# Kernel tuning notes

Measured on AMD Instinct MI355X. Metric: run time of the kernel, lower is better.

## Reference

```python
import jax, jax.numpy as jnp
import numpy as np

B, NUM_RX, NUM_CHIRPS, SAMPLES = 16, 4, 64, 256
D_BINS, R_BINS = 64, 256


def _conv3d(x, w, b, pad):
    y = jax.lax.conv_general_dilated(x, w, (1, 1, 1), pad,
                                     dimension_numbers=('NCDHW', 'OIDHW', 'NCDHW'))
    return y + b[None, :, None, None, None]


def _conv2d(x, w, b, pad):
    y = jax.lax.conv_general_dilated(x, w, (1, 1), pad,
                                     dimension_numbers=('NCHW', 'OIHW', 'NCHW'))
    return y + b[None, :, None, None]


def _bn2(x, s, t):
    return x * s[None, :, None, None] + t[None, :, None, None]


def _bn3(x, s, t):
    return x * s[None, :, None, None, None] + t[None, :, None, None, None]


def _upsample_bilinear_ac(x, oh, ow):
    # torch Upsample(mode='bilinear', align_corners=True)
    _, _, h, w = x.shape
    ph = jnp.linspace(0.0, h - 1.0, oh)
    pw = jnp.linspace(0.0, w - 1.0, ow)
    h0 = jnp.clip(jnp.floor(ph).astype(jnp.int32), 0, h - 1)
    h1 = jnp.clip(h0 + 1, 0, h - 1)
    fh = ph - h0
    w0 = jnp.clip(jnp.floor(pw).astype(jnp.int32), 0, w - 1)
    w1 = jnp.clip(w0 + 1, 0, w - 1)
    fw = pw - w0
    x = x[:, :, h0, :] * (1.0 - fh)[None, None, :, None] + x[:, :, h1, :] * fh[None, None, :, None]
    x = x[:, :, :, w0] * (1.0 - fw) + x[:, :, :, w1] * fw
    return x


def setup_inputs() -> dict:
    ks = iter(jax.random.split(jax.random.key(0), 80))

    def nrm(shape, s=0.05):
        return s * jax.random.normal(next(ks), shape, dtype=jnp.float32)

    inp = {'x': jax.random.normal(next(ks), (B, NUM_RX, NUM_CHIRPS, SAMPLES, 2), dtype=jnp.float32)}

    def conv(name, shape):
        inp[name + '_w'] = nrm(shape)
        inp[name + '_b'] = nrm((shape[0],))

    def bn(name, n):  # BatchNorm in inference form folded to scale/shift
        inp[name + '_s'] = 1.0 + nrm((n,), 0.1)
        inp[name + '_t'] = nrm((n,), 0.1)

    conv('tc1', (16, 2, 1, 1, 3)); bn('tc1', 16)
    conv('tc2', (32, 16, 1, 1, 3)); bn('tc2', 32)
    conv('rx', (32, 32, NUM_RX, 1, 1)); bn('rx', 32)
    conv('cc1', (64, 32 * NUM_CHIRPS, 3, 3)); bn('cc1', 64)
    conv('cc2', (64, 64, 3, 3)); bn('cc2', 64)
    conv('rd1', (128, 64, 3, 3)); bn('rd1', 128)
    conv('rd2', (128, 128, 3, 3)); bn('rd2', 128)
    conv('up1', (64, 128, 3, 3)); bn('up1', 64)
    conv('up2', (32, 64, 3, 3)); bn('up2', 32)
    conv('up3', (1, 32, 1, 1))
    inp['wr'] = jax.random.normal(next(ks), (SAMPLES, R_BINS, 2), dtype=jnp.float32)
    inp['wd'] = jax.random.normal(next(ks), (NUM_CHIRPS, D_BINS, 2), dtype=jnp.float32)
    return inp


def reference(x, tc1_w, tc1_b, tc1_s, tc1_t, tc2_w, tc2_b, tc2_s, tc2_t,
              rx_w, rx_b, rx_s, rx_t, cc1_w, cc1_b, cc1_s, cc1_t,
              cc2_w, cc2_b, cc2_s, cc2_t, rd1_w, rd1_b, rd1_s, rd1_t,
              rd2_w, rd2_b, rd2_s, rd2_t, up1_w, up1_b, up1_s, up1_t,
              up2_w, up2_b, up2_s, up2_t, up3_w, up3_b, wr, wd):
    r = jax.nn.relu
    p3 = [(0, 0), (0, 0), (1, 1)]
    p2 = [(1, 1), (1, 1)]
    h = jnp.transpose(x, (0, 4, 1, 2, 3))                      # [B,2,RX,C,S]
    h = r(_bn3(_conv3d(h, tc1_w, tc1_b, p3), tc1_s, tc1_t))
    h = r(_bn3(_conv3d(h, tc2_w, tc2_b, p3), tc2_s, tc2_t))
    h = r(_bn3(_conv3d(h, rx_w, rx_b, [(0, 0)] * 3), rx_s, rx_t))[:, :, 0]  # [B,32,C,S]
    h = h.reshape(h.shape[0], -1, SAMPLES)[:, :, None, :]      # [B,32*C,1,S]
    h = r(_bn2(_conv2d(h, cc1_w, cc1_b, p2), cc1_s, cc1_t))
    h = r(_bn2(_conv2d(h, cc2_w, cc2_b, p2), cc2_s, cc2_t))
    h = r(_bn2(_conv2d(h, rd1_w, rd1_b, p2), rd1_s, rd1_t))
    h = r(_bn2(_conv2d(h, rd2_w, rd2_b, p2), rd2_s, rd2_t))
    h = _upsample_bilinear_ac(h, D_BINS, R_BINS)               # [B,128,D,R]
    h = r(_bn2(_conv2d(h, up1_w, up1_b, p2), up1_s, up1_t))
    h = r(_bn2(_conv2d(h, up2_w, up2_b, p2), up2_s, up2_t))
    h = jax.nn.sigmoid(_conv2d(h, up3_w, up3_b, [(0, 0), (0, 0)]))  # [B,1,D,R]
    # learnable_fft (input is real: x_imag = 0), loops -> two batched matmuls
    xr = h[:, 0]                                               # [B,D,R]
    rr = jnp.einsum('bcs,sr->bcr', xr, wr[:, :, 0])            # range DFT, real
    ri = jnp.einsum('bcs,sr->bcr', xr, wr[:, :, 1])            # range DFT, imag
    rdr = jnp.einsum('bcr,cd->bdr', rr, wd[:, :, 0]) - jnp.einsum('bcr,cd->bdr', ri, wd[:, :, 1])
    rdi = jnp.einsum('bcr,cd->bdr', rr, wd[:, :, 1]) + jnp.einsum('bcr,cd->bdr', ri, wd[:, :, 0])
    mag = jnp.sqrt(rdr * rdr + rdi * rdi) / (NUM_CHIRPS * SAMPLES)
    out = jnp.clip(h + 0.1 * mag[:, None], 0.0, 1.0)
    return jnp.transpose(out, (0, 2, 3, 1))                    # [B,D,R,1]
```

## Files before the change

kernel.cpp:

```cpp
#include <hip/hip_runtime.h>
#include <math.h>

#define OFF_A      0u
#define OFF_P      8388608u
#define OFF_WCC1   10485760u
#define OFF_BCC1   11010048u
#define OFF_WCC2   11010112u
#define OFF_BCC2   11026496u
#define OFF_WRD1   11026560u
#define OFF_BRD1   11059328u
#define OFF_WRD2   11059456u
#define OFF_BRD2   11124992u
#define OFF_WUP1   11125120u
#define OFF_BUP1   11223424u
#define OFF_WUP2   11223488u
#define OFF_BUP2   11346368u
#define OFF_WRX    11346400u
#define OFF_W1F    11350496u
#define OFF_B1F    11350592u
#define OFF_W2F    11350608u
#define OFF_B2F    11352144u
#define OFF_BRXF   11352176u
#define OFF_R      0u
#define OFF_U1     524288u
#define OFF_H      1310720u

__device__ __forceinline__ void fma4(float4& a, const float4& x, float w) {
  a.x = fmaf(x.x, w, a.x); a.y = fmaf(x.y, w, a.y);
  a.z = fmaf(x.z, w, a.z); a.w = fmaf(x.w, w, a.w);
}

__global__ __launch_bounds__(256) void k_repack(
    const float* __restrict__ tc1_w, const float* __restrict__ tc1_b, const float* __restrict__ tc1_s, const float* __restrict__ tc1_t,
    const float* __restrict__ tc2_w, const float* __restrict__ tc2_b, const float* __restrict__ tc2_s, const float* __restrict__ tc2_t,
    const float* __restrict__ rx_w, const float* __restrict__ rx_b, const float* __restrict__ rx_s, const float* __restrict__ rx_t,
    const float* __restrict__ cc1_w, const float* __restrict__ cc1_b, const float* __restrict__ cc1_s, const float* __restrict__ cc1_t,
    const float* __restrict__ cc2_w, const float* __restrict__ cc2_b, const float* __restrict__ cc2_s, const float* __restrict__ cc2_t,
    const float* __restrict__ rd1_w, const float* __restrict__ rd1_b, const float* __restrict__ rd1_s, const float* __restrict__ rd1_t,
    const float* __restrict__ rd2_w, const float* __restrict__ rd2_b, const float* __restrict__ rd2_s, const float* __restrict__ rd2_t,
    const float* __restrict__ up1_w, const float* __restrict__ up1_b, const float* __restrict__ up1_s, const float* __restrict__ up1_t,
    const float* __restrict__ up2_w, const float* __restrict__ up2_b, const float* __restrict__ up2_s, const float* __restrict__ up2_t,
    float* __restrict__ ws)
{
  const int tid = blockIdx.x * blockDim.x + threadIdx.x;
  const int nth = gridDim.x * blockDim.x;

  for (int i = tid; i < 96; i += nth) ws[OFF_W1F + i] = tc1_w[i] * tc1_s[i/6];
  for (int i = tid; i < 16; i += nth) ws[OFF_B1F + i] = tc1_b[i]*tc1_s[i] + tc1_t[i];
  for (int i = tid; i < 1536; i += nth) {
    int oc = i & 31, r = i >> 5, k = r % 3, ic = r / 3;
    ws[OFF_W2F + i] = tc2_w[oc*48 + ic*3 + k] * tc2_s[oc];
  }
  for (int i = tid; i < 32; i += nth) ws[OFF_B2F + i] = tc2_b[i]*tc2_s[i] + tc2_t[i];
  for (int i = tid; i < 4096; i += nth) {
    int oc = i & 31, ic = (i >> 5) & 31, rxi = i >> 10;
    ws[OFF_WRX + i] = rx_w[(oc*32 + ic)*4 + rxi] * rx_s[oc];
  }
  for (int i = tid; i < 32; i += nth) ws[OFF_BRXF + i] = rx_b[i]*rx_s[i] + rx_t[i];

  for (int i = tid; i < 2048*64*4; i += nth) {
    int k = i & 3, oc = (i >> 2) & 63, c2 = i >> 8;
    ws[OFF_WCC1 + i] = (k < 3) ? cc1_w[((oc*2048 + c2)*3 + 1)*3 + k] * cc1_s[oc] : 0.f;
  }
  for (int i = tid; i < 64; i += nth) ws[OFF_BCC1 + i] = cc1_b[i]*cc1_s[i] + cc1_t[i];

  for (int i = tid; i < 64*64*4; i += nth) {
    int k = i & 3, oc = (i >> 2) & 63, ic = i >> 8;
    ws[OFF_WCC2 + i] = (k < 3) ? cc2_w[((oc*64 + ic)*3 + 1)*3 + k] * cc2_s[oc] : 0.f;
  }
  for (int i = tid; i < 64; i += nth) ws[OFF_BCC2 + i] = cc2_b[i]*cc2_s[i] + cc2_t[i];

  for (int i = tid; i < 64*128*4; i += nth) {
    int k = i & 3, oc = (i >> 2) & 127, ic = i >> 9;
    ws[OFF_WRD1 + i] = (k < 3) ? rd1_w[((oc*64 + ic)*3 + 1)*3 + k] * rd1_s[oc] : 0.f;
  }
  for (int i = tid; i < 128; i += nth) ws[OFF_BRD1 + i] = rd1_b[i]*rd1_s[i] + rd1_t[i];

  for (int i = tid; i < 128*128*4; i += nth) {
    int k = i & 3, oc = (i >> 2) & 127, ic = i >> 9;
    ws[OFF_WRD2 + i] = (k < 3) ? rd2_w[((oc*128 + ic)*3 + 1)*3 + k] * rd2_s[oc] : 0.f;
  }
  for (int i = tid; i < 128; i += nth) ws[OFF_BRD2 + i] = rd2_b[i]*rd2_s[i] + rd2_t[i];

  for (int i = tid; i < 3*128*64*4; i += nth) {
    int k = i & 3, oc = (i >> 2) & 63, ic = (i >> 8) & 127, v = i >> 15;
    float val = 0.f;
    if (k < 3) {
      const int m = (v == 0) ? 6 : (v == 1) ? 7 : 3;
      float a = 0.f;
      for (int kh = 0; kh < 3; ++kh)
        if ((m >> kh) & 1) a += up1_w[((oc*128 + ic)*3 + kh)*3 + k];
      val = a * up1_s[oc];
    }
    ws[OFF_WUP1 + i] = val;
  }
  for (int i = tid; i < 64; i += nth) ws[OFF_BUP1 + i] = up1_b[i]*up1_s[i] + up1_t[i];

  for (int i = tid; i < 5*3*64*32*4; i += nth) {
    int k = i & 3, oc = (i >> 2) & 31, ic = (i >> 7) & 63, t = i >> 13;
    int src = t % 3, v = t / 3;
    float val = 0.f;
    if (k < 3) {
      const int MASKS[15] = {2,4,0,  1,6,0,  0,7,0,  0,3,4,  0,1,2};
      const int m = MASKS[v*3 + src];
      float a = 0.f;
      for (int kh = 0; kh < 3; ++kh)
        if ((m >> kh) & 1) a += up2_w[((oc*64 + ic)*3 + kh)*3 + k];
      val = a * up2_s[oc];
    }
    ws[OFF_WUP2 + i] = val;
  }
  for (int i = tid; i < 32; i += nth) ws[OFF_BUP2 + i] = up2_b[i]*up2_s[i] + up2_t[i];
}

__global__ __launch_bounds__(256, 4) void k_front(
    const float* __restrict__ x, const float* __restrict__ ws, float* __restrict__ A)
{
  __shared__ float t1s[16][258];
  const int tid = threadIdx.x;
  const int b = blockIdx.x >> 6, chirp = blockIdx.x & 63;
  const int s = tid;

  if (tid < 32) { int o = tid & 15; int c = (tid >> 4) ? 257 : 0; t1s[o][c] = 0.f; }

  const float* w1f  = ws + OFF_W1F;
  const float* b1f  = ws + OFF_B1F;
  const float* w2f  = ws + OFF_W2F;
  const float* b2f  = ws + OFF_B2F;
  const float* wrxf = ws + OFF_WRX;
  const float* brxf = ws + OFF_BRXF;

  float acc[32];
  #pragma unroll
  for (int j = 0; j < 32; ++j) acc[j] = 0.f;

  #pragma unroll 1
  for (int rxi = 0; rxi < 4; ++rxi) {
    {
      const float2* xb2 = (const float2*)(x + ((size_t)(((b*4 + rxi)*64 + chirp)*256) << 1));
      float2 xm = xb2[s];
      float2 xl = xb2[(s == 0) ? 0 : (s - 1)];
      float2 xr = xb2[(s == 255) ? 255 : (s + 1)];
      if (s == 0)   { xl.x = 0.f; xl.y = 0.f; }
      if (s == 255) { xr.x = 0.f; xr.y = 0.f; }
      #pragma unroll 4
      for (int o = 0; o < 16; ++o) {
        const float* w = w1f + o*6;
        float v = b1f[o];
        v = fmaf(xl.x, w[0], v);
        v = fmaf(xm.x, w[1], v);
        v = fmaf(xr.x, w[2], v);
        v = fmaf(xl.y, w[3], v);
        v = fmaf(xm.y, w[4], v);
        v = fmaf(xr.y, w[5], v);
        t1s[o][s+1] = fmaxf(v, 0.f);
      }
    }
    __syncthreads();

    float t2[32];
    #pragma unroll
    for (int j = 0; j < 32; ++j) t2[j] = b2f[j];
    #pragma unroll 2
    for (int ic = 0; ic < 16; ++ic) {
      float tl = t1s[ic][s];
      float tm = t1s[ic][s+1];
      float tr = t1s[ic][s+2];
      const float* w = w2f + ic*96;
      #pragma unroll
      for (int oc = 0; oc < 32; ++oc)
        t2[oc] = fmaf(tl, w[oc], fmaf(tm, w[32+oc], fmaf(tr, w[64+oc], t2[oc])));
    }
    #pragma unroll
    for (int j = 0; j < 32; ++j) t2[j] = fmaxf(t2[j], 0.f);

    const float* wr0 = wrxf + rxi*1024;
    #pragma unroll 4
    for (int ic = 0; ic < 32; ++ic) {
      float tv = t2[ic];
      const float* w = wr0 + ic*32;
      #pragma unroll
      for (int oc = 0; oc < 32; ++oc)
        acc[oc] = fmaf(tv, w[oc], acc[oc]);
    }
    __syncthreads();
  }

  #pragma unroll 4
  for (int oc = 0; oc < 32; ++oc) {
    float v = fmaxf(acc[oc] + brxf[oc], 0.f);
    A[(size_t)((b*2048 + oc*64 + chirp)*256) + s] = v;
  }
}

__global__ __launch_bounds__(256) void k_cc1(
    const float* __restrict__ A, const float* __restrict__ wp, float* __restrict__ P)
{
  __shared__ __align__(16) float As[256][36];
  const int tid = threadIdx.x;
  const int ks = blockIdx.x & 7;
  const int stile = (blockIdx.x >> 3) & 7;
  const int b = blockIdx.x >> 6;
  const int s0 = stile * 32;
  const int oc = tid & 63;
  const int sg = tid >> 6;
  const int cbase = ks * 256;
  const float4* w4 = (const float4*)wp;

  for (int i = tid; i < 256*36; i += 256) {
    int c = i / 36, si = i - c*36;
    int sA = s0 - 1 + si;
    float v = 0.f;
    if (si < 34 && sA >= 0 && sA < 256)
      v = A[(size_t)(b*2048 + cbase + c)*256 + sA];
    As[c][si] = v;
  }
  __syncthreads();

  const int sb = sg * 8;
  float4 acc0 = make_float4(0.f,0.f,0.f,0.f);
  float4 acc1 = make_float4(0.f,0.f,0.f,0.f);
  #pragma unroll 4
  for (int c = 0; c < 256; ++c) {
    float4 w = w4[(size_t)(cbase + c)*64 + oc];
    float4 a0 = *(const float4*)&As[c][sb];
    float4 a1 = *(const float4*)&As[c][sb + 4];
    float2 a2 = *(const float2*)&As[c][sb + 8];
    acc0.x = fmaf(a0.x,w.x, fmaf(a0.y,w.y, fmaf(a0.z,w.z, acc0.x)));
    acc0.y = fmaf(a0.y,w.x, fmaf(a0.z,w.y, fmaf(a0.w,w.z, acc0.y)));
    acc0.z = fmaf(a0.z,w.x, fmaf(a0.w,w.y, fmaf(a1.x,w.z, acc0.z)));
    acc0.w = fmaf(a0.w,w.x, fmaf(a1.x,w.y, fmaf(a1.y,w.z, acc0.w)));
    acc1.x = fmaf(a1.x,w.x, fmaf(a1.y,w.y, fmaf(a1.z,w.z, acc1.x)));
    acc1.y = fmaf(a1.y,w.x, fmaf(a1.z,w.y, fmaf(a1.w,w.z, acc1.y)));
    acc1.z = fmaf(a1.z,w.x, fmaf(a1.w,w.y, fmaf(a2.x,w.z, acc1.z)));
    acc1.w = fmaf(a1.w,w.x, fmaf(a2.x,w.y, fmaf(a2.y,w.z, acc1.w)));
  }
  float* Pk = P + ((size_t)(ks*16 + b)*256)*64;
  int s = s0 + sb;
  Pk[(size_t)(s+0)*64 + oc] = acc0.x;
  Pk[(size_t)(s+1)*64 + oc] = acc0.y;
  Pk[(size_t)(s+2)*64 + oc] = acc0.z;
  Pk[(size_t)(s+3)*64 + oc] = acc0.w;
  Pk[(size_t)(s+4)*64 + oc] = acc1.x;
  Pk[(size_t)(s+5)*64 + oc] = acc1.y;
  Pk[(size_t)(s+6)*64 + oc] = acc1.z;
  Pk[(size_t)(s+7)*64 + oc] = acc1.w;
}

__global__ __launch_bounds__(256) void k_mid(
    const float* __restrict__ P, const float* __restrict__ bcc1,
    const float* __restrict__ wcc2, const float* __restrict__ bcc2,
    const float* __restrict__ wrd1, const float* __restrict__ brd1,
    const float* __restrict__ wrd2, const float* __restrict__ brd2,
    float* __restrict__ R)
{
  __shared__ float c1s[14][64];
  __shared__ float c2s[14][64];
  __shared__ float r1s[10][128];
  const int tid = threadIdx.x;
  const int b = blockIdx.x >> 5;
  const int s0 = (blockIdx.x & 31) * 8;
  const float4* wc2 = (const float4*)wcc2;
  const float4* wr1 = (const float4*)wrd1;
  const float4* wr2 = (const float4*)wrd2;

  for (int i = tid; i < 14*64; i += 256) {
    int si = i >> 6, ic = i & 63;
    int sA = s0 - 3 + si;
    float v = 0.f;
    if (sA >= 0 && sA < 256) {
      float a = bcc1[ic];
      #pragma unroll
      for (int ksp = 0; ksp < 8; ++ksp)
        a += P[((size_t)(ksp*16 + b)*256 + sA)*64 + ic];
      v = fmaxf(a, 0.f);
    }
    c1s[si][ic] = v;
  }
  __syncthreads();

  {
    const int g = tid >> 6, oc = tid & 63;
    if (g < 3) {
      float4 acc;
      float bb = bcc2[oc];
      acc = make_float4(bb, bb, bb, bb);
      for (int ic = 0; ic < 64; ++ic) {
        float4 w = wc2[ic*64 + oc];
        float c0 = c1s[g*4+0][ic], c1 = c1s[g*4+1][ic], c2 = c1s[g*4+2][ic];
        float c3 = c1s[g*4+3][ic], c4 = c1s[g*4+4][ic], c5 = c1s[g*4+5][ic];
        acc.x = fmaf(c0,w.x, fmaf(c1,w.y, fmaf(c2,w.z, acc.x)));
        acc.y = fmaf(c1,w.x, fmaf(c2,w.y, fmaf(c3,w.z, acc.y)));
        acc.z = fmaf(c2,w.x, fmaf(c3,w.y, fmaf(c4,w.z, acc.z)));
        acc.w = fmaf(c3,w.x, fmaf(c4,w.y, fmaf(c5,w.z, acc.w)));
      }
      c2s[g*4+0][oc] = fmaxf(acc.x, 0.f);
      c2s[g*4+1][oc] = fmaxf(acc.y, 0.f);
      c2s[g*4+2][oc] = fmaxf(acc.z, 0.f);
      c2s[g*4+3][oc] = fmaxf(acc.w, 0.f);
    } else {
      int k = tid - 192;
      c2s[12][k] = 0.f;
      c2s[13][k] = 0.f;
    }
  }
  __syncthreads();

  for (int it = tid; it < 384; it += 256) {
    const int oc = it & 127, g = it >> 7;
    float4 acc;
    float bb = brd1[oc];
    acc = make_float4(bb, bb, bb, bb);
    for (int ic = 0; ic < 64; ++ic) {
      float4 w = wr1[ic*128 + oc];
      float c0 = c2s[g*4+0][ic], c1 = c2s[g*4+1][ic], c2 = c2s[g*4+2][ic];
      float c3 = c2s[g*4+3][ic], c4 = c2s[g*4+4][ic], c5 = c2s[g*4+5][ic];
      acc.x = fmaf(c0,w.x, fmaf(c1,w.y, fmaf(c2,w.z, acc.x)));
      acc.y = fmaf(c1,w.x, fmaf(c2,w.y, fmaf(c3,w.z, acc.y)));
      acc.z = fmaf(c2,w.x, fmaf(c3,w.y, fmaf(c4,w.z, acc.z)));
      acc.w = fmaf(c3,w.x, fmaf(c4,w.y, fmaf(c5,w.z, acc.w)));
    }
    r1s[g*4+0][oc] = fmaxf(acc.x, 0.f);
    r1s[g*4+1][oc] = fmaxf(acc.y, 0.f);
    if (g < 2) {
      r1s[g*4+2][oc] = fmaxf(acc.z, 0.f);
      r1s[g*4+3][oc] = fmaxf(acc.w, 0.f);
    }
  }
  __syncthreads();

  {
    const int g = tid >> 7, oc = tid & 127;
    float4 acc;
    float bb = brd2[oc];
    acc = make_float4(bb, bb, bb, bb);
    for (int ic = 0; ic < 128; ++ic) {
      float4 w = wr2[ic*128 + oc];
      float c0 = r1s[g*4+0][ic], c1 = r1s[g*4+1][ic], c2 = r1s[g*4+2][ic];
      float c3 = r1s[g*4+3][ic], c4 = r1s[g*4+4][ic], c5 = r1s[g*4+5][ic];
      acc.x = fmaf(c0,w.x, fmaf(c1,w.y, fmaf(c2,w.z, acc.x)));
      acc.y = fmaf(c1,w.x, fmaf(c2,w.y, fmaf(c3,w.z, acc.y)));
      acc.z = fmaf(c2,w.x, fmaf(c3,w.y, fmaf(c4,w.z, acc.z)));
      acc.w = fmaf(c3,w.x, fmaf(c4,w.y, fmaf(c5,w.z, acc.w)));
    }
    int s = s0 + g*4;
    R[((size_t)b*256 + s+0)*128 + oc] = fmaxf(acc.x, 0.f);
    R[((size_t)b*256 + s+1)*128 + oc] = fmaxf(acc.y, 0.f);
    R[((size_t)b*256 + s+2)*128 + oc] = fmaxf(acc.z, 0.f);
    R[((size_t)b*256 + s+3)*128 + oc] = fmaxf(acc.w, 0.f);
  }
}

__global__ __launch_bounds__(192) void k_up1(
    const float* __restrict__ R, const float* __restrict__ wup1, const float* __restrict__ bup1,
    float* __restrict__ U1)
{
  __shared__ float Rs[10][128];
  const int tid = threadIdx.x;
  const int b = blockIdx.x >> 5;
  const int s0 = (blockIdx.x & 31) * 8;
  for (int i = tid; i < 10*128; i += 192) {
    int si = i >> 7, ic = i & 127;
    int sA = s0 - 1 + si;
    Rs[si][ic] = (sA >= 0 && sA < 256) ? R[((size_t)b*256 + sA)*128 + ic] : 0.f;
  }
  __syncthreads();
  const int vi = tid >> 6, oc = tid & 63;
  const float4* w4 = (const float4*)wup1;
  float acc[8];
  float bb = bup1[oc];
  #pragma unroll
  for (int j = 0; j < 8; ++j) acc[j] = bb;
  for (int ic = 0; ic < 128; ++ic) {
    float4 w = w4[(vi*128 + ic)*64 + oc];
    float r0 = Rs[0][ic], r1 = Rs[1][ic], r2 = Rs[2][ic], r3 = Rs[3][ic], r4 = Rs[4][ic];
    float r5 = Rs[5][ic], r6 = Rs[6][ic], r7 = Rs[7][ic], r8 = Rs[8][ic], r9 = Rs[9][ic];
    acc[0] = fmaf(r0,w.x, fmaf(r1,w.y, fmaf(r2,w.z, acc[0])));
    acc[1] = fmaf(r1,w.x, fmaf(r2,w.y, fmaf(r3,w.z, acc[1])));
    acc[2] = fmaf(r2,w.x, fmaf(r3,w.y, fmaf(r4,w.z, acc[2])));
    acc[3] = fmaf(r3,w.x, fmaf(r4,w.y, fmaf(r5,w.z, acc[3])));
    acc[4] = fmaf(r4,w.x, fmaf(r5,w.y, fmaf(r6,w.z, acc[4])));
    acc[5] = fmaf(r5,w.x, fmaf(r6,w.y, fmaf(r7,w.z, acc[5])));
    acc[6] = fmaf(r6,w.x, fmaf(r7,w.y, fmaf(r8,w.z, acc[6])));
    acc[7] = fmaf(r7,w.x, fmaf(r8,w.y, fmaf(r9,w.z, acc[7])));
  }
  #pragma unroll
  for (int j = 0; j < 8; ++j)
    U1[((size_t)(b*3 + vi)*256 + s0 + j)*64 + oc] = fmaxf(acc[j], 0.f);
}

__global__ __launch_bounds__(192) void k_up2(
    const float* __restrict__ U1, const float* __restrict__ wup2, const float* __restrict__ bup2,
    const float* __restrict__ up3_w, const float* __restrict__ up3_b,
    float* __restrict__ H)
{
  __shared__ float u1s[3][10][64];
  __shared__ float u2s[5][32][9];
  const int tid = threadIdx.x;
  const int b = blockIdx.x >> 5;
  const int s0 = (blockIdx.x & 31) * 8;
  for (int i = tid; i < 3*10*64; i += 192) {
    int v = i / 640, r = i - v*640, si = r >> 6, ic = r & 63;
    int sA = s0 - 1 + si;
    u1s[v][si][ic] = (sA >= 0 && sA < 256) ? U1[((size_t)(b*3 + v)*256 + sA)*64 + ic] : 0.f;
  }
  __syncthreads();
  if (tid < 160) {
    const int v = tid >> 5, oc = tid & 31;
    const float4* w4 = (const float4*)wup2;
    float acc[8];
    float bb = bup2[oc];
    #pragma unroll
    for (int j = 0; j < 8; ++j) acc[j] = bb;
    for (int src = 0; src < 3; ++src)
      for (int ic = 0; ic < 64; ++ic) {
        float4 w = w4[((v*3 + src)*64 + ic)*32 + oc];
        float r0 = u1s[src][0][ic], r1 = u1s[src][1][ic], r2 = u1s[src][2][ic];
        float r3 = u1s[src][3][ic], r4 = u1s[src][4][ic], r5 = u1s[src][5][ic];
        float r6 = u1s[src][6][ic], r7 = u1s[src][7][ic], r8 = u1s[src][8][ic];
        float r9 = u1s[src][9][ic];
        acc[0] = fmaf(r0,w.x, fmaf(r1,w.y, fmaf(r2,w.z, acc[0])));
        acc[1] = fmaf(r1,w.x, fmaf(r2,w.y, fmaf(r3,w.z, acc[1])));
        acc[2] = fmaf(r2,w.x, fmaf(r3,w.y, fmaf(r4,w.z, acc[2])));
        acc[3] = fmaf(r3,w.x, fmaf(r4,w.y, fmaf(r5,w.z, acc[3])));
        acc[4] = fmaf(r4,w.x, fmaf(r5,w.y, fmaf(r6,w.z, acc[4])));
        acc[5] = fmaf(r5,w.x, fmaf(r6,w.y, fmaf(r7,w.z, acc[5])));
        acc[6] = fmaf(r6,w.x, fmaf(r7,w.y, fmaf(r8,w.z, acc[6])));
        acc[7] = fmaf(r7,w.x, fmaf(r8,w.y, fmaf(r9,w.z, acc[7])));
      }
    #pragma unroll
    for (int j = 0; j < 8; ++j) u2s[v][oc][j] = fmaxf(acc[j], 0.f);
  }
  __syncthreads();
  if (tid < 40) {
    int v = tid >> 3, j = tid & 7;
    float a = up3_b[0];
    for (int ic = 0; ic < 32; ++ic)
      a = fmaf(u2s[v][ic][j], up3_w[ic], a);
    H[(size_t)(b*5 + v)*256 + s0 + j] = 1.f / (1.f + expf(-a));
  }
}

__global__ __launch_bounds__(64) void k_spec(
    const float* __restrict__ H, const float* __restrict__ wr, const float* __restrict__ wd,
    float* __restrict__ out)
{
  __shared__ float hs[5][256];
  __shared__ float S0[64], S1[64];
  __shared__ float wds[4][64][2];
  const int tid = threadIdx.x;
  const int b = blockIdx.x >> 2;
  const int rt = blockIdx.x & 3;
  for (int i = tid; i < 1280; i += 64) hs[i >> 8][i & 255] = H[(size_t)b*1280 + i];
  {
    float a0 = 0.f, a1 = 0.f;
    for (int c = 2; c <= 61; ++c) {
      a0 += wd[(c*64 + tid)*2 + 0];
      a1 += wd[(c*64 + tid)*2 + 1];
    }
    S0[tid] = a0; S1[tid] = a1;
  }
  for (int i = tid; i < 512; i += 64) {
    int row = i >> 7, rem = i & 127, d = rem >> 1, comp = rem & 1;
    int c = (row < 2) ? row : (60 + row);
    wds[row][d][comp] = wd[(c*64 + d)*2 + comp];
  }
  __syncthreads();
  const int r = rt*64 + tid;
  float rr0=0,rr1=0,rr2=0,rr3=0,rr4=0, ri0=0,ri1=0,ri2=0,ri3=0,ri4=0;
  const float2* wr2p = (const float2*)wr;
  for (int s = 0; s < 256; ++s) {
    float2 w = wr2p[s*256 + r];
    float h0 = hs[0][s], h1 = hs[1][s], h2 = hs[2][s], h3 = hs[3][s], h4 = hs[4][s];
    rr0 = fmaf(h0, w.x, rr0); ri0 = fmaf(h0, w.y, ri0);
    rr1 = fmaf(h1, w.x, rr1); ri1 = fmaf(h1, w.y, ri1);
    rr2 = fmaf(h2, w.x, rr2); ri2 = fmaf(h2, w.y, ri2);
    rr3 = fmaf(h3, w.x, rr3); ri3 = fmaf(h3, w.y, ri3);
    rr4 = fmaf(h4, w.x, rr4); ri4 = fmaf(h4, w.y, ri4);
  }
  for (int d = 0; d < 64; ++d) {
    float w0r = wds[0][d][0], w0i = wds[0][d][1];
    float w1r = wds[1][d][0], w1i = wds[1][d][1];
    float w2r = wds[2][d][0], w2i = wds[2][d][1];
    float w3r = wds[3][d][0], w3i = wds[3][d][1];
    float s0v = S0[d], s1v = S1[d];
    float rdr = rr0*w0r + rr1*w1r + rr2*s0v + rr3*w2r + rr4*w3r
              - ri0*w0i - ri1*w1i - ri2*s1v - ri3*w2i - ri4*w3i;
    float rdi = rr0*w0i + rr1*w1i + rr2*s1v + rr3*w2i + rr4*w3i
              + ri0*w0r + ri1*w1r + ri2*s0v + ri3*w2r + ri4*w3r;
    float mag = sqrtf(rdr*rdr + rdi*rdi) * (1.0f / 16384.0f);
    int v = (d == 0) ? 0 : (d == 1) ? 1 : (d <= 61) ? 2 : ((d == 62) ? 3 : 4);
    float o = hs[v][r] + 0.1f * mag;
    out[(size_t)b*16384 + d*256 + r] = fminf(fmaxf(o, 0.f), 1.f);
  }
}

extern "C" void kernel_launch(void* const* d_in, const int* in_sizes, int n_in,
                              void* d_out, int out_size, void* d_ws, size_t ws_size,
                              hipStream_t stream)
{
  const float* x     = (const float*)d_in[0];
  const float* tc1_w = (const float*)d_in[1];  const float* tc1_b = (const float*)d_in[2];
  const float* tc1_s = (const float*)d_in[3];  const float* tc1_t = (const float*)d_in[4];
  const float* tc2_w = (const float*)d_in[5];  const float* tc2_b = (const float*)d_in[6];
  const float* tc2_s = (const float*)d_in[7];  const float* tc2_t = (const float*)d_in[8];
  const float* rx_w  = (const float*)d_in[9];  const float* rx_b  = (const float*)d_in[10];
  const float* rx_s  = (const float*)d_in[11]; const float* rx_t  = (const float*)d_in[12];
  const float* cc1_w = (const float*)d_in[13]; const float* cc1_b = (const float*)d_in[14];
  const float* cc1_s = (const float*)d_in[15]; const float* cc1_t = (const float*)d_in[16];
  const float* cc2_w = (const float*)d_in[17]; const float* cc2_b = (const float*)d_in[18];
  const float* cc2_s = (const float*)d_in[19]; const float* cc2_t = (const float*)d_in[20];
  const float* rd1_w = (const float*)d_in[21]; const float* rd1_b = (const float*)d_in[22];
  const float* rd1_s = (const float*)d_in[23]; const float* rd1_t = (const float*)d_in[24];
  const float* rd2_w = (const float*)d_in[25]; const float* rd2_b = (const float*)d_in[26];
  const float* rd2_s = (const float*)d_in[27]; const float* rd2_t = (const float*)d_in[28];
  const float* up1_w = (const float*)d_in[29]; const float* up1_b = (const float*)d_in[30];
  const float* up1_s = (const float*)d_in[31]; const float* up1_t = (const float*)d_in[32];
  const float* up2_w = (const float*)d_in[33]; const float* up2_b = (const float*)d_in[34];
  const float* up2_s = (const float*)d_in[35]; const float* up2_t = (const float*)d_in[36];
  const float* up3_w = (const float*)d_in[37]; const float* up3_b = (const float*)d_in[38];
  const float* wr    = (const float*)d_in[39];
  const float* wd    = (const float*)d_in[40];
  float* ws  = (float*)d_ws;
  float* out = (float*)d_out;

  k_repack<<<1024, 256, 0, stream>>>(tc1_w, tc1_b, tc1_s, tc1_t,
                                     tc2_w, tc2_b, tc2_s, tc2_t,
                                     rx_w, rx_b, rx_s, rx_t,
                                     cc1_w, cc1_b, cc1_s, cc1_t,
                                     cc2_w, cc2_b, cc2_s, cc2_t,
                                     rd1_w, rd1_b, rd1_s, rd1_t,
                                     rd2_w, rd2_b, rd2_s, rd2_t,
                                     up1_w, up1_b, up1_s, up1_t,
                                     up2_w, up2_b, up2_s, up2_t, ws);
  k_front<<<1024, 256, 0, stream>>>(x, ws, ws + OFF_A);
  k_cc1<<<1024, 256, 0, stream>>>(ws + OFF_A, ws + OFF_WCC1, ws + OFF_P);
  k_mid<<<512, 256, 0, stream>>>(ws + OFF_P, ws + OFF_BCC1,
                                 ws + OFF_WCC2, ws + OFF_BCC2,
                                 ws + OFF_WRD1, ws + OFF_BRD1,
                                 ws + OFF_WRD2, ws + OFF_BRD2, ws + OFF_R);
  k_up1<<<512, 192, 0, stream>>>(ws + OFF_R, ws + OFF_WUP1, ws + OFF_BUP1, ws + OFF_U1);
  k_up2<<<512, 192, 0, stream>>>(ws + OFF_U1, ws + OFF_WUP2, ws + OFF_BUP2, up3_w, up3_b, ws + OFF_H);
  k_spec<<<64, 64, 0, stream>>>(ws + OFF_H, wr, wd, out);
}
```

Measured before the change: 392.7 us.

## Restructure front, cc1, mid, up and spectral kernels; fuse up1/up2

Several kernels are reworked together. k_front splits each chirp across two 128-thread blocks with halo recompute. k_cc1 drops the padded weight layout, moves to 128 threads each computing 4 positions by 4 output channels, and writes float4 stores. k_mid transposes its shared tiles so activations load as vectors. k_up1 and k_up2 are fused into one kernel that keeps the intermediate in shared memory, removing a launch and a global round trip. k_spec goes to 256 threads, splitting the range DFT over sample quarters with a shared-memory reduction, to raise parallelism in the tail kernel. In exchange these add more shared memory, extra halo work and new code paths that risk errors.

```diff
diff --git a/kernel.cpp b/kernel.cpp
--- a/kernel.cpp
+++ b/kernel.cpp
@@ -4,26 +4,25 @@
 #define OFF_A      0u
 #define OFF_P      8388608u
 #define OFF_WCC1   10485760u
-#define OFF_BCC1   11010048u
-#define OFF_WCC2   11010112u
-#define OFF_BCC2   11026496u
-#define OFF_WRD1   11026560u
-#define OFF_BRD1   11059328u
-#define OFF_WRD2   11059456u
-#define OFF_BRD2   11124992u
-#define OFF_WUP1   11125120u
-#define OFF_BUP1   11223424u
-#define OFF_WUP2   11223488u
-#define OFF_BUP2   11346368u
-#define OFF_WRX    11346400u
-#define OFF_W1F    11350496u
-#define OFF_B1F    11350592u
-#define OFF_W2F    11350608u
-#define OFF_B2F    11352144u
-#define OFF_BRXF   11352176u
+#define OFF_BCC1   10878976u
+#define OFF_WCC2   10879040u
+#define OFF_BCC2   10895424u
+#define OFF_WRD1   10895488u
+#define OFF_BRD1   10928256u
+#define OFF_WRD2   10928384u
+#define OFF_BRD2   10993920u
+#define OFF_WUP1   10994048u
+#define OFF_BUP1   11092352u
+#define OFF_WUP2   11092416u
+#define OFF_BUP2   11215296u
+#define OFF_WRX    11215328u
+#define OFF_W1F    11219424u
+#define OFF_B1F    11219520u
+#define OFF_W2F    11219536u
+#define OFF_B2F    11221072u
+#define OFF_BRXF   11221104u
 #define OFF_R      0u
-#define OFF_U1     524288u
-#define OFF_H      1310720u
+#define OFF_H      524288u
 
 __device__ __forceinline__ void fma4(float4& a, const float4& x, float w) {
   a.x = fmaf(x.x, w, a.x); a.y = fmaf(x.y, w, a.y);
@@ -58,70 +57,88 @@
   }
   for (int i = tid; i < 32; i += nth) ws[OFF_BRXF + i] = rx_b[i]*rx_s[i] + rx_t[i];
 
-  for (int i = tid; i < 2048*64*4; i += nth) {
-    int k = i & 3, oc = (i >> 2) & 63, c2 = i >> 8;
-    ws[OFF_WCC1 + i] = (k < 3) ? cc1_w[((oc*2048 + c2)*3 + 1)*3 + k] * cc1_s[oc] : 0.f;
+  for (int i = tid; i < 2048*192; i += nth) {
+    int c = i / 192, r = i - c*192, k = r >> 6, oc = r & 63;
+    ws[OFF_WCC1 + i] = cc1_w[((oc*2048 + c)*3 + 1)*3 + k] * cc1_s[oc];
   }
   for (int i = tid; i < 64; i += nth) ws[OFF_BCC1 + i] = cc1_b[i]*cc1_s[i] + cc1_t[i];
 
-  for (int i = tid; i < 64*64*4; i += nth) {
-    int k = i & 3, oc = (i >> 2) & 63, ic = i >> 8;
-    ws[OFF_WCC2 + i] = (k < 3) ? cc2_w[((oc*64 + ic)*3 + 1)*3 + k] * cc2_s[oc] : 0.f;
+  for (int i = tid; i < 64*64; i += nth) {
+    int oc = i & 63, ic = i >> 6;
+    float4 v;
+    v.x = cc2_w[(oc*64 + ic)*9 + 3] * cc2_s[oc];
+    v.y = cc2_w[(oc*64 + ic)*9 + 4] * cc2_s[oc];
+    v.z = cc2_w[(oc*64 + ic)*9 + 5] * cc2_s[oc];
+    v.w = 0.f;
+    ((float4*)(ws + OFF_WCC2))[i] = v;
   }
   for (int i = tid; i < 64; i += nth) ws[OFF_BCC2 + i] = cc2_b[i]*cc2_s[i] + cc2_t[i];
 
-  for (int i = tid; i < 64*128*4; i += nth) {
-    int k = i & 3, oc = (i >> 2) & 127, ic = i >> 9;
-    ws[OFF_WRD1 + i] = (k < 3) ? rd1_w[((oc*64 + ic)*3 + 1)*3 + k] * rd1_s[oc] : 0.f;
+  for (int i = tid; i < 64*128; i += nth) {
+    int oc = i & 127, ic = i >> 7;
+    float4 v;
+    v.x = rd1_w[(oc*64 + ic)*9 + 3] * rd1_s[oc];
+    v.y = rd1_w[(oc*64 + ic)*9 + 4] * rd1_s[oc];
+    v.z = rd1_w[(oc*64 + ic)*9 + 5] * rd1_s[oc];
+    v.w = 0.f;
+    ((float4*)(ws + OFF_WRD1))[i] = v;
   }
   for (int i = tid; i < 128; i += nth) ws[OFF_BRD1 + i] = rd1_b[i]*rd1_s[i] + rd1_t[i];
 
-  for (int i = tid; i < 128*128*4; i += nth) {
-    int k = i & 3, oc = (i >> 2) & 127, ic = i >> 9;
-    ws[OFF_WRD2 + i] = (k < 3) ? rd2_w[((oc*128 + ic)*3 + 1)*3 + k] * rd2_s[oc] : 0.f;
+  for (int i = tid; i < 128*128; i += nth) {
+    int oc = i & 127, ic = i >> 7;
+    float4 v;
+    v.x = rd2_w[(oc*128 + ic)*9 + 3] * rd2_s[oc];
+    v.y = rd2_w[(oc*128 + ic)*9 + 4] * rd2_s[oc];
+    v.z = rd2_w[(oc*128 + ic)*9 + 5] * rd2_s[oc];
+    v.w = 0.f;
+    ((float4*)(ws + OFF_WRD2))[i] = v;
   }
   for (int i = tid; i < 128; i += nth) ws[OFF_BRD2 + i] = rd2_b[i]*rd2_s[i] + rd2_t[i];
 
-  for (int i = tid; i < 3*128*64*4; i += nth) {
-    int k = i & 3, oc = (i >> 2) & 63, ic = (i >> 8) & 127, v = i >> 15;
-    float val = 0.f;
-    if (k < 3) {
-      const int m = (v == 0) ? 6 : (v == 1) ? 7 : 3;
-      float a = 0.f;
-      for (int kh = 0; kh < 3; ++kh)
-        if ((m >> kh) & 1) a += up1_w[((oc*128 + ic)*3 + kh)*3 + k];
-      val = a * up1_s[oc];
-    }
-    ws[OFF_WUP1 + i] = val;
+  for (int i = tid; i < 3*128*64; i += nth) {
+    int oc = i & 63, ic = (i >> 6) & 127, v = i >> 13;
+    const int m = (v == 0) ? 6 : (v == 1) ? 7 : 3;
+    float4 o = make_float4(0.f, 0.f, 0.f, 0.f);
+    for (int kh = 0; kh < 3; ++kh)
+      if ((m >> kh) & 1) {
+        o.x += up1_w[((oc*128 + ic)*3 + kh)*3 + 0];
+        o.y += up1_w[((oc*128 + ic)*3 + kh)*3 + 1];
+        o.z += up1_w[((oc*128 + ic)*3 + kh)*3 + 2];
+      }
+    o.x *= up1_s[oc]; o.y *= up1_s[oc]; o.z *= up1_s[oc];
+    ((float4*)(ws + OFF_WUP1))[i] = o;
   }
   for (int i = tid; i < 64; i += nth) ws[OFF_BUP1 + i] = up1_b[i]*up1_s[i] + up1_t[i];
 
-  for (int i = tid; i < 5*3*64*32*4; i += nth) {
-    int k = i & 3, oc = (i >> 2) & 31, ic = (i >> 7) & 63, t = i >> 13;
+  for (int i = tid; i < 5*3*64*32; i += nth) {
+    int oc = i & 31, ic = (i >> 5) & 63, t = i >> 11;
     int src = t % 3, v = t / 3;
-    float val = 0.f;
-    if (k < 3) {
-      const int MASKS[15] = {2,4,0,  1,6,0,  0,7,0,  0,3,4,  0,1,2};
-      const int m = MASKS[v*3 + src];
-      float a = 0.f;
-      for (int kh = 0; kh < 3; ++kh)
-        if ((m >> kh) & 1) a += up2_w[((oc*64 + ic)*3 + kh)*3 + k];
-      val = a * up2_s[oc];
-    }
-    ws[OFF_WUP2 + i] = val;
+    const int MASKS[15] = {2,4,0,  1,6,0,  0,7,0,  0,3,4,  0,1,2};
+    const int m = MASKS[v*3 + src];
+    float4 o = make_float4(0.f, 0.f, 0.f, 0.f);
+    for (int kh = 0; kh < 3; ++kh)
+      if ((m >> kh) & 1) {
+        o.x += up2_w[((oc*64 + ic)*3 + kh)*3 + 0];
+        o.y += up2_w[((oc*64 + ic)*3 + kh)*3 + 1];
+        o.z += up2_w[((oc*64 + ic)*3 + kh)*3 + 2];
+      }
+    o.x *= up2_s[oc]; o.y *= up2_s[oc]; o.z *= up2_s[oc];
+    ((float4*)(ws + OFF_WUP2))[i] = o;
   }
   for (int i = tid; i < 32; i += nth) ws[OFF_BUP2 + i] = up2_b[i]*up2_s[i] + up2_t[i];
 }
 
-__global__ __launch_bounds__(256, 4) void k_front(
+__global__ __launch_bounds__(128, 4) void k_front(
     const float* __restrict__ x, const float* __restrict__ ws, float* __restrict__ A)
 {
-  __shared__ float t1s[16][258];
+  __shared__ float t1s[16][132];
   const int tid = threadIdx.x;
-  const int b = blockIdx.x >> 6, chirp = blockIdx.x & 63;
-  const int s = tid;
-
-  if (tid < 32) { int o = tid & 15; int c = (tid >> 4) ? 257 : 0; t1s[o][c] = 0.f; }
+  const int b = blockIdx.x >> 7;
+  const int chirp = (blockIdx.x >> 1) & 63;
+  const int h = blockIdx.x & 1;
+  const int hs0 = h << 7;
+  const int s = hs0 + tid;
 
   const float* w1f  = ws + OFF_W1F;
   const float* b1f  = ws + OFF_B1F;
@@ -136,24 +153,28 @@
 
   #pragma unroll 1
   for (int rxi = 0; rxi < 4; ++rxi) {
-    {
-      const float2* xb2 = (const float2*)(x + ((size_t)(((b*4 + rxi)*64 + chirp)*256) << 1));
-      float2 xm = xb2[s];
-      float2 xl = xb2[(s == 0) ? 0 : (s - 1)];
-      float2 xr = xb2[(s == 255) ? 255 : (s + 1)];
-      if (s == 0)   { xl.x = 0.f; xl.y = 0.f; }
-      if (s == 255) { xr.x = 0.f; xr.y = 0.f; }
-      #pragma unroll 4
-      for (int o = 0; o < 16; ++o) {
-        const float* w = w1f + o*6;
-        float v = b1f[o];
-        v = fmaf(xl.x, w[0], v);
-        v = fmaf(xm.x, w[1], v);
-        v = fmaf(xr.x, w[2], v);
-        v = fmaf(xl.y, w[3], v);
-        v = fmaf(xm.y, w[4], v);
-        v = fmaf(xr.y, w[5], v);
-        t1s[o][s+1] = fmaxf(v, 0.f);
+    const float2* xb2 = (const float2*)(x + ((size_t)(((b*4 + rxi)*64 + chirp)*256) << 1));
+    for (int j = tid; j < 130; j += 128) {
+      int sc = hs0 - 1 + j;
+      if (sc < 0 || sc > 255) {
+        #pragma unroll
+        for (int o = 0; o < 16; ++o) t1s[o][j] = 0.f;
+      } else {
+        float2 xm = xb2[sc];
+        float2 xl = (sc == 0)   ? make_float2(0.f, 0.f) : xb2[sc-1];
+        float2 xr = (sc == 255) ? make_float2(0.f, 0.f) : xb2[sc+1];
+        #pragma unroll 4
+        for (int o = 0; o < 16; ++o) {
+          const float* w = w1f + o*6;
+          float v = b1f[o];
+          v = fmaf(xl.x, w[0], v);
+          v = fmaf(xm.x, w[1], v);
+          v = fmaf(xr.x, w[2], v);
+          v = fmaf(xl.y, w[3], v);
+          v = fmaf(xm.y, w[4], v);
+          v = fmaf(xr.y, w[5], v);
+          t1s[o][j] = fmaxf(v, 0.f);
+        }
       }
     }
     __syncthreads();
@@ -163,9 +184,9 @@
     for (int j = 0; j < 32; ++j) t2[j] = b2f[j];
     #pragma unroll 2
     for (int ic = 0; ic < 16; ++ic) {
-      float tl = t1s[ic][s];
-      float tm = t1s[ic][s+1];
-      float tr = t1s[ic][s+2];
+      float tl = t1s[ic][tid];
+      float tm = t1s[ic][tid+1];
+      float tr = t1s[ic][tid+2];
       const float* w = w2f + ic*96;
       #pragma unroll
       for (int oc = 0; oc < 32; ++oc)
@@ -193,7 +214,7 @@
   }
 }
 
-__global__ __launch_bounds__(256) void k_cc1(
+__global__ __launch_bounds__(128) void k_cc1(
     const float* __restrict__ A, const float* __restrict__ wp, float* __restrict__ P)
 {
   __shared__ __align__(16) float As[256][36];
@@ -202,12 +223,12 @@
   const int stile = (blockIdx.x >> 3) & 7;
   const int b = blockIdx.x >> 6;
   const int s0 = stile * 32;
-  const int oc = tid & 63;
-  const int sg = tid >> 6;
+  const int ocq = tid & 15;
+  const int sg = tid >> 4;
+  const int sb = sg * 4;
   const int cbase = ks * 256;
-  const float4* w4 = (const float4*)wp;
-
-  for (int i = tid; i < 256*36; i += 256) {
+
+  for (int i = tid; i < 256*36; i += 128) {
     int c = i / 36, si = i - c*36;
     int sA = s0 - 1 + si;
     float v = 0.f;
@@ -217,34 +238,28 @@
   }
   __syncthreads();
 
-  const int sb = sg * 8;
-  float4 acc0 = make_float4(0.f,0.f,0.f,0.f);
-  float4 acc1 = make_float4(0.f,0.f,0.f,0.f);
+  float4 acc[4];
+  #pragma unroll
+  for (int j = 0; j < 4; ++j) acc[j] = make_float4(0.f,0.f,0.f,0.f);
+
+  const float4* w4 = (const float4*)wp;
   #pragma unroll 4
   for (int c = 0; c < 256; ++c) {
-    float4 w = w4[(size_t)(cbase + c)*64 + oc];
+    const float4* wc = w4 + (size_t)(cbase + c)*48 + ocq;
+    float4 wk0 = wc[0];
+    float4 wk1 = wc[16];
+    float4 wk2 = wc[32];
     float4 a0 = *(const float4*)&As[c][sb];
-    float4 a1 = *(const float4*)&As[c][sb + 4];
-    float2 a2 = *(const float2*)&As[c][sb + 8];
-    acc0.x = fmaf(a0.x,w.x, fmaf(a0.y,w.y, fmaf(a0.z,w.z, acc0.x)));
-    acc0.y = fmaf(a0.y,w.x, fmaf(a0.z,w.y, fmaf(a0.w,w.z, acc0.y)));
-    acc0.z = fmaf(a0.z,w.x, fmaf(a0.w,w.y, fmaf(a1.x,w.z, acc0.z)));
-    acc0.w = fmaf(a0.w,w.x, fmaf(a1.x,w.y, fmaf(a1.y,w.z, acc0.w)));
-    acc1.x = fmaf(a1.x,w.x, fmaf(a1.y,w.y, fmaf(a1.z,w.z, acc1.x)));
-    acc1.y = fmaf(a1.y,w.x, fmaf(a1.z,w.y, fmaf(a1.w,w.z, acc1.y)));
-    acc1.z = fmaf(a1.z,w.x, fmaf(a1.w,w.y, fmaf(a2.x,w.z, acc1.z)));
-    acc1.w = fmaf(a1.w,w.x, fmaf(a2.x,w.y, fmaf(a2.y,w.z, acc1.w)));
+    float2 a1 = *(const float2*)&As[c][sb + 4];
+    fma4(acc[0], wk0, a0.x); fma4(acc[0], wk1, a0.y); fma4(acc[0], wk2, a0.z);
+    fma4(acc[1], wk0, a0.y); fma4(acc[1], wk1, a0.z); fma4(acc[1], wk2, a0.w);
+    fma4(acc[2], wk0, a0.z); fma4(acc[2], wk1, a0.w); fma4(acc[2], wk2, a1.x);
+    fma4(acc[3], wk0, a0.w); fma4(acc[3], wk1, a1.x); fma4(acc[3], wk2, a1.y);
   }
   float* Pk = P + ((size_t)(ks*16 + b)*256)*64;
-  int s = s0 + sb;
-  Pk[(size_t)(s+0)*64 + oc] = acc0.x;
-  Pk[(size_t)(s+1)*64 + oc] = acc0.y;
-  Pk[(size_t)(s+2)*64 + oc] = acc0.z;
-  Pk[(size_t)(s+3)*64 + oc] = acc0.w;
-  Pk[(size_t)(s+4)*64 + oc] = acc1.x;
-  Pk[(size_t)(s+5)*64 + oc] = acc1.y;
-  Pk[(size_t)(s+6)*64 + oc] = acc1.z;
-  Pk[(size_t)(s+7)*64 + oc] = acc1.w;
+  #pragma unroll
+  for (int j = 0; j < 4; ++j)
+    *(float4*)&Pk[(size_t)(s0 + sb + j)*64 + ocq*4] = acc[j];
 }
 
 __global__ __launch_bounds__(256) void k_mid(
@@ -254,9 +269,9 @@
     const float* __restrict__ wrd2, const float* __restrict__ brd2,
     float* __restrict__ R)
 {
-  __shared__ float c1s[14][64];
-  __shared__ float c2s[14][64];
-  __shared__ float r1s[10][128];
+  __shared__ __align__(16) float c1s[64][20];
+  __shared__ __align__(16) float c2s[64][20];
+  __shared__ __align__(16) float r1s[128][12];
   const int tid = threadIdx.x;
   const int b = blockIdx.x >> 5;
   const int s0 = (blockIdx.x & 31) * 8;
@@ -264,8 +279,8 @@
   const float4* wr1 = (const float4*)wrd1;
   const float4* wr2 = (const float4*)wrd2;
 
-  for (int i = tid; i < 14*64; i += 256) {
-    int si = i >> 6, ic = i & 63;
+  for (int i = tid; i < 64*14; i += 256) {
+    int ic = i & 63, si = i >> 6;
     int sA = s0 - 3 + si;
     float v = 0.f;
     if (sA >= 0 && sA < 256) {
@@ -275,73 +290,68 @@
         a += P[((size_t)(ksp*16 + b)*256 + sA)*64 + ic];
       v = fmaxf(a, 0.f);
     }
-    c1s[si][ic] = v;
+    c1s[ic][si] = v;
   }
   __syncthreads();
 
   {
     const int g = tid >> 6, oc = tid & 63;
     if (g < 3) {
-      float4 acc;
       float bb = bcc2[oc];
-      acc = make_float4(bb, bb, bb, bb);
+      float4 acc = make_float4(bb, bb, bb, bb);
       for (int ic = 0; ic < 64; ++ic) {
         float4 w = wc2[ic*64 + oc];
-        float c0 = c1s[g*4+0][ic], c1 = c1s[g*4+1][ic], c2 = c1s[g*4+2][ic];
-        float c3 = c1s[g*4+3][ic], c4 = c1s[g*4+4][ic], c5 = c1s[g*4+5][ic];
-        acc.x = fmaf(c0,w.x, fmaf(c1,w.y, fmaf(c2,w.z, acc.x)));
-        acc.y = fmaf(c1,w.x, fmaf(c2,w.y, fmaf(c3,w.z, acc.y)));
-        acc.z = fmaf(c2,w.x, fmaf(c3,w.y, fmaf(c4,w.z, acc.z)));
-        acc.w = fmaf(c3,w.x, fmaf(c4,w.y, fmaf(c5,w.z, acc.w)));
+        float4 ca = *(const float4*)&c1s[ic][g*4];
+        float2 cb = *(const float2*)&c1s[ic][g*4 + 4];
+        acc.x = fmaf(ca.x,w.x, fmaf(ca.y,w.y, fmaf(ca.z,w.z, acc.x)));
+        acc.y = fmaf(ca.y,w.x, fmaf(ca.z,w.y, fmaf(ca.w,w.z, acc.y)));
+        acc.z = fmaf(ca.z,w.x, fmaf(ca.w,w.y, fmaf(cb.x,w.z, acc.z)));
+        acc.w = fmaf(ca.w,w.x, fmaf(cb.x,w.y, fmaf(cb.y,w.z, acc.w)));
       }
-      c2s[g*4+0][oc] = fmaxf(acc.x, 0.f);
-      c2s[g*4+1][oc] = fmaxf(acc.y, 0.f);
-      c2s[g*4+2][oc] = fmaxf(acc.z, 0.f);
-      c2s[g*4+3][oc] = fmaxf(acc.w, 0.f);
+      c2s[oc][g*4+0] = fmaxf(acc.x, 0.f);
+      c2s[oc][g*4+1] = fmaxf(acc.y, 0.f);
+      c2s[oc][g*4+2] = fmaxf(acc.z, 0.f);
+      c2s[oc][g*4+3] = fmaxf(acc.w, 0.f);
     } else {
-      int k = tid - 192;
-      c2s[12][k] = 0.f;
-      c2s[13][k] = 0.f;
+      int oc2 = tid - 192;
+      c2s[oc2][12] = 0.f;
+      c2s[oc2][13] = 0.f;
     }
   }
   __syncthreads();
 
   for (int it = tid; it < 384; it += 256) {
     const int oc = it & 127, g = it >> 7;
-    float4 acc;
     float bb = brd1[oc];
-    acc = make_float4(bb, bb, bb, bb);
+    float4 acc = make_float4(bb, bb, bb, bb);
     for (int ic = 0; ic < 64; ++ic) {
       float4 w = wr1[ic*128 + oc];
-      float c0 = c2s[g*4+0][ic], c1 = c2s[g*4+1][ic], c2 = c2s[g*4+2][ic];
-      float c3 = c2s[g*4+3][ic], c4 = c2s[g*4+4][ic], c5 = c2s[g*4+5][ic];
-      acc.x = fmaf(c0,w.x, fmaf(c1,w.y, fmaf(c2,w.z, acc.x)));
-      acc.y = fmaf(c1,w.x, fmaf(c2,w.y, fmaf(c3,w.z, acc.y)));
-      acc.z = fmaf(c2,w.x, fmaf(c3,w.y, fmaf(c4,w.z, acc.z)));
-      acc.w = fmaf(c3,w.x, fmaf(c4,w.y, fmaf(c5,w.z, acc.w)));
-    }
-    r1s[g*4+0][oc] = fmaxf(acc.x, 0.f);
-    r1s[g*4+1][oc] = fmaxf(acc.y, 0.f);
-    if (g < 2) {
-      r1s[g*4+2][oc] = fmaxf(acc.z, 0.f);
-      r1s[g*4+3][oc] = fmaxf(acc.w, 0.f);
-    }
+      float4 ca = *(const float4*)&c2s[ic][g*4];
+      float2 cb = *(const float2*)&c2s[ic][g*4 + 4];
+      acc.x = fmaf(ca.x,w.x, fmaf(ca.y,w.y, fmaf(ca.z,w.z, acc.x)));
+      acc.y = fmaf(ca.y,w.x, fmaf(ca.z,w.y, fmaf(ca.w,w.z, acc.y)));
+      acc.z = fmaf(ca.z,w.x, fmaf(ca.w,w.y, fmaf(cb.x,w.z, acc.z)));
+      acc.w = fmaf(ca.w,w.x, fmaf(cb.x,w.y, fmaf(cb.y,w.z, acc.w)));
+    }
+    if (g*4 + 0 < 12) r1s[oc][g*4+0] = fmaxf(acc.x, 0.f);
+    if (g*4 + 1 < 12) r1s[oc][g*4+1] = fmaxf(acc.y, 0.f);
+    if (g*4 + 2 < 12) r1s[oc][g*4+2] = fmaxf(acc.z, 0.f);
+    if (g*4 + 3 < 12) r1s[oc][g*4+3] = fmaxf(acc.w, 0.f);
   }
   __syncthreads();
 
   {
     const int g = tid >> 7, oc = tid & 127;
-    float4 acc;
     float bb = brd2[oc];
-    acc = make_float4(bb, bb, bb, bb);
+    float4 acc = make_float4(bb, bb, bb, bb);
     for (int ic = 0; ic < 128; ++ic) {
       float4 w = wr2[ic*128 + oc];
-      float c0 = r1s[g*4+0][ic], c1 = r1s[g*4+1][ic], c2 = r1s[g*4+2][ic];
-      float c3 = r1s[g*4+3][ic], c4 = r1s[g*4+4][ic], c5 = r1s[g*4+5][ic];
-      acc.x = fmaf(c0,w.x, fmaf(c1,w.y, fmaf(c2,w.z, acc.x)));
-      acc.y = fmaf(c1,w.x, fmaf(c2,w.y, fmaf(c3,w.z, acc.y)));
-      acc.z = fmaf(c2,w.x, fmaf(c3,w.y, fmaf(c4,w.z, acc.z)));
-      acc.w = fmaf(c3,w.x, fmaf(c4,w.y, fmaf(c5,w.z, acc.w)));
+      float4 ca = *(const float4*)&r1s[ic][g*4];
+      float2 cb = *(const float2*)&r1s[ic][g*4 + 4];
+      acc.x = fmaf(ca.x,w.x, fmaf(ca.y,w.y, fmaf(ca.z,w.z, acc.x)));
+      acc.y = fmaf(ca.y,w.x, fmaf(ca.z,w.y, fmaf(ca.w,w.z, acc.y)));
+      acc.z = fmaf(ca.z,w.x, fmaf(ca.w,w.y, fmaf(cb.x,w.z, acc.z)));
+      acc.w = fmaf(ca.w,w.x, fmaf(cb.x,w.y, fmaf(cb.y,w.z, acc.w)));
     }
     int s = s0 + g*4;
     R[((size_t)b*256 + s+0)*128 + oc] = fmaxf(acc.x, 0.f);
@@ -351,87 +361,88 @@
   }
 }
 
-__global__ __launch_bounds__(192) void k_up1(
-    const float* __restrict__ R, const float* __restrict__ wup1, const float* __restrict__ bup1,
-    float* __restrict__ U1)
-{
-  __shared__ float Rs[10][128];
-  const int tid = threadIdx.x;
-  const int b = blockIdx.x >> 5;
-  const int s0 = (blockIdx.x & 31) * 8;
-  for (int i = tid; i < 10*128; i += 192) {
-    int si = i >> 7, ic = i & 127;
-    int sA = s0 - 1 + si;
-    Rs[si][ic] = (sA >= 0 && sA < 256) ? R[((size_t)b*256 + sA)*128 + ic] : 0.f;
-  }
-  __syncthreads();
-  const int vi = tid >> 6, oc = tid & 63;
-  const float4* w4 = (const float4*)wup1;
-  float acc[8];
-  float bb = bup1[oc];
-  #pragma unroll
-  for (int j = 0; j < 8; ++j) acc[j] = bb;
-  for (int ic = 0; ic < 128; ++ic) {
-    float4 w = w4[(vi*128 + ic)*64 + oc];
-    float r0 = Rs[0][ic], r1 = Rs[1][ic], r2 = Rs[2][ic], r3 = Rs[3][ic], r4 = Rs[4][ic];
-    float r5 = Rs[5][ic], r6 = Rs[6][ic], r7 = Rs[7][ic], r8 = Rs[8][ic], r9 = Rs[9][ic];
-    acc[0] = fmaf(r0,w.x, fmaf(r1,w.y, fmaf(r2,w.z, acc[0])));
-    acc[1] = fmaf(r1,w.x, fmaf(r2,w.y, fmaf(r3,w.z, acc[1])));
-    acc[2] = fmaf(r2,w.x, fmaf(r3,w.y, fmaf(r4,w.z, acc[2])));
-    acc[3] = fmaf(r3,w.x, fmaf(r4,w.y, fmaf(r5,w.z, acc[3])));
-    acc[4] = fmaf(r4,w.x, fmaf(r5,w.y, fmaf(r6,w.z, acc[4])));
-    acc[5] = fmaf(r5,w.x, fmaf(r6,w.y, fmaf(r7,w.z, acc[5])));
-    acc[6] = fmaf(r6,w.x, fmaf(r7,w.y, fmaf(r8,w.z, acc[6])));
-    acc[7] = fmaf(r7,w.x, fmaf(r8,w.y, fmaf(r9,w.z, acc[7])));
-  }
-  #pragma unroll
-  for (int j = 0; j < 8; ++j)
-    U1[((size_t)(b*3 + vi)*256 + s0 + j)*64 + oc] = fmaxf(acc[j], 0.f);
-}
-
-__global__ __launch_bounds__(192) void k_up2(
-    const float* __restrict__ U1, const float* __restrict__ wup2, const float* __restrict__ bup2,
+__global__ __launch_bounds__(192) void k_up(
+    const float* __restrict__ R,
+    const float* __restrict__ wup1, const float* __restrict__ bup1,
+    const float* __restrict__ wup2, const float* __restrict__ bup2,
     const float* __restrict__ up3_w, const float* __restrict__ up3_b,
     float* __restrict__ H)
 {
-  __shared__ float u1s[3][10][64];
+  __shared__ __align__(16) float Rs[128][12];
+  __shared__ __align__(16) float u1s[3][64][12];
   __shared__ float u2s[5][32][9];
   const int tid = threadIdx.x;
   const int b = blockIdx.x >> 5;
   const int s0 = (blockIdx.x & 31) * 8;
-  for (int i = tid; i < 3*10*64; i += 192) {
-    int v = i / 640, r = i - v*640, si = r >> 6, ic = r & 63;
-    int sA = s0 - 1 + si;
-    u1s[v][si][ic] = (sA >= 0 && sA < 256) ? U1[((size_t)(b*3 + v)*256 + sA)*64 + ic] : 0.f;
-  }
-  __syncthreads();
-  if (tid < 160) {
-    const int v = tid >> 5, oc = tid & 31;
+
+  for (int i = tid; i < 128*12; i += 192) {
+    int ic = i & 127, si = i >> 7;
+    int sA = s0 - 2 + si;
+    Rs[ic][si] = (sA >= 0 && sA < 256) ? R[((size_t)b*256 + sA)*128 + ic] : 0.f;
+  }
+  __syncthreads();
+
+  if (tid < 96) {
+    const int vi = tid >> 5, ocp = tid & 31;
+    const int oc0 = ocp*2, oc1 = ocp*2 + 1;
+    const float4* w4 = (const float4*)wup1;
+    float a0[10], a1[10];
+    float bb0 = bup1[oc0], bb1 = bup1[oc1];
+    #pragma unroll
+    for (int p = 0; p < 10; ++p) { a0[p] = bb0; a1[p] = bb1; }
+    for (int ic = 0; ic < 128; ++ic) {
+      float4 w0 = w4[(vi*128 + ic)*64 + oc0];
+      float4 w1 = w4[(vi*128 + ic)*64 + oc1];
+      float4 ra = *(const float4*)&Rs[ic][0];
+      float4 rb = *(const float4*)&Rs[ic][4];
+      float4 rc = *(const float4*)&Rs[ic][8];
+      float r[12] = {ra.x,ra.y,ra.z,ra.w, rb.x,rb.y,rb.z,rb.w, rc.x,rc.y,rc.z,rc.w};
+      #pragma unroll
+      for (int p = 0; p < 10; ++p) {
+        a0[p] = fmaf(r[p],w0.x, fmaf(r[p+1],w0.y, fmaf(r[p+2],w0.z, a0[p])));
+        a1[p] = fmaf(r[p],w1.x, fmaf(r[p+1],w1.y, fmaf(r[p+2],w1.z, a1[p])));
+      }
+    }
+    #pragma unroll
+    for (int p = 0; p < 10; ++p) {
+      u1s[vi][oc0][p] = fmaxf(a0[p], 0.f);
+      u1s[vi][oc1][p] = fmaxf(a1[p], 0.f);
+    }
+    u1s[vi][oc0][10] = 0.f; u1s[vi][oc0][11] = 0.f;
+    u1s[vi][oc1][10] = 0.f; u1s[vi][oc1][11] = 0.f;
+  }
+  __syncthreads();
+
+  if (tid < 80) {
+    const int v = tid >> 4, ocp = tid & 15;
+    const int oc0 = ocp*2, oc1 = ocp*2 + 1;
     const float4* w4 = (const float4*)wup2;
-    float acc[8];
-    float bb = bup2[oc];
-    #pragma unroll
-    for (int j = 0; j < 8; ++j) acc[j] = bb;
+    float a0[8], a1[8];
+    float bb0 = bup2[oc0], bb1 = bup2[oc1];
+    #pragma unroll
+    for (int p = 0; p < 8; ++p) { a0[p] = bb0; a1[p] = bb1; }
     for (int src = 0; src < 3; ++src)
       for (int ic = 0; ic < 64; ++ic) {
-        float4 w = w4[((v*3 + src)*64 + ic)*32 + oc];
-        float r0 = u1s[src][0][ic], r1 = u1s[src][1][ic], r2 = u1s[src][2][ic];
-        float r3 = u1s[src][3][ic], r4 = u1s[src][4][ic], r5 = u1s[src][5][ic];
-        float r6 = u1s[src][6][ic], r7 = u1s[src][7][ic], r8 = u1s[src][8][ic];
-        float r9 = u1s[src][9][ic];
-        acc[0] = fmaf(r0,w.x, fmaf(r1,w.y, fmaf(r2,w.z, acc[0])));
-        acc[1] = fmaf(r1,w.x, fmaf(r2,w.y, fmaf(r3,w.z, acc[1])));
-        acc[2] = fmaf(r2,w.x, fmaf(r3,w.y, fmaf(r4,w.z, acc[2])));
-        acc[3] = fmaf(r3,w.x, fmaf(r4,w.y, fmaf(r5,w.z, acc[3])));
-        acc[4] = fmaf(r4,w.x, fmaf(r5,w.y, fmaf(r6,w.z, acc[4])));
-        acc[5] = fmaf(r5,w.x, fmaf(r6,w.y, fmaf(r7,w.z, acc[5])));
-        acc[6] = fmaf(r6,w.x, fmaf(r7,w.y, fmaf(r8,w.z, acc[6])));
-        acc[7] = fmaf(r7,w.x, fmaf(r8,w.y, fmaf(r9,w.z, acc[7])));
+        float4 w0 = w4[((v*3 + src)*64 + ic)*32 + oc0];
+        float4 w1 = w4[((v*3 + src)*64 + ic)*32 + oc1];
+        float4 ua = *(const float4*)&u1s[src][ic][0];
+        float4 ub = *(const float4*)&u1s[src][ic][4];
+        float2 uc = *(const float2*)&u1s[src][ic][8];
+        float r[10] = {ua.x,ua.y,ua.z,ua.w, ub.x,ub.y,ub.z,ub.w, uc.x,uc.y};
+        #pragma unroll
+        for (int p = 0; p < 8; ++p) {
+          a0[p] = fmaf(r[p],w0.x, fmaf(r[p+1],w0.y, fmaf(r[p+2],w0.z, a0[p])));
+          a1[p] = fmaf(r[p],w1.x, fmaf(r[p+1],w1.y, fmaf(r[p+2],w1.z, a1[p])));
+        }
       }
     #pragma unroll
-    for (int j = 0; j < 8; ++j) u2s[v][oc][j] = fmaxf(acc[j], 0.f);
-  }
-  __syncthreads();
+    for (int p = 0; p < 8; ++p) {
+      u2s[v][oc0][p] = fmaxf(a0[p], 0.f);
+      u2s[v][oc1][p] = fmaxf(a1[p], 0.f);
+    }
+  }
+  __syncthreads();
+
   if (tid < 40) {
     int v = tid >> 3, j = tid & 7;
     float a = up3_b[0];
@@ -441,53 +452,74 @@
   }
 }
 
-__global__ __launch_bounds__(64) void k_spec(
+__global__ __launch_bounds__(256) void k_spec(
     const float* __restrict__ H, const float* __restrict__ wr, const float* __restrict__ wd,
     float* __restrict__ out)
 {
   __shared__ float hs[5][256];
   __shared__ float S0[64], S1[64];
   __shared__ float wds[4][64][2];
+  __shared__ float ps[4][64][11];
   const int tid = threadIdx.x;
   const int b = blockIdx.x >> 2;
   const int rt = blockIdx.x & 3;
-  for (int i = tid; i < 1280; i += 64) hs[i >> 8][i & 255] = H[(size_t)b*1280 + i];
-  {
+
+  for (int i = tid; i < 1280; i += 256) hs[i >> 8][i & 255] = H[(size_t)b*1280 + i];
+  if (tid < 64) {
+    const float2* wd2 = (const float2*)wd;
     float a0 = 0.f, a1 = 0.f;
     for (int c = 2; c <= 61; ++c) {
-      a0 += wd[(c*64 + tid)*2 + 0];
-      a1 += wd[(c*64 + tid)*2 + 1];
+      float2 v = wd2[c*64 + tid];
+      a0 += v.x; a1 += v.y;
     }
     S0[tid] = a0; S1[tid] = a1;
   }
-  for (int i = tid; i < 512; i += 64) {
+  for (int i = tid; i < 512; i += 256) {
     int row = i >> 7, rem = i & 127, d = rem >> 1, comp = rem & 1;
     int c = (row < 2) ? row : (60 + row);
     wds[row][d][comp] = wd[(c*64 + d)*2 + comp];
   }
   __syncthreads();
-  const int r = rt*64 + tid;
-  float rr0=0,rr1=0,rr2=0,rr3=0,rr4=0, ri0=0,ri1=0,ri2=0,ri3=0,ri4=0;
+
+  const int rl = tid & 63;
+  const int r = rt*64 + rl;
+  const int sq = tid >> 6;
+  float rr[5] = {0,0,0,0,0}, ri[5] = {0,0,0,0,0};
   const float2* wr2p = (const float2*)wr;
-  for (int s = 0; s < 256; ++s) {
+  for (int s = sq*64; s < sq*64 + 64; ++s) {
     float2 w = wr2p[s*256 + r];
-    float h0 = hs[0][s], h1 = hs[1][s], h2 = hs[2][s], h3 = hs[3][s], h4 = hs[4][s];
-    rr0 = fmaf(h0, w.x, rr0); ri0 = fmaf(h0, w.y, ri0);
-    rr1 = fmaf(h1, w.x, rr1); ri1 = fmaf(h1, w.y, ri1);
-    rr2 = fmaf(h2, w.x, rr2); ri2 = fmaf(h2, w.y, ri2);
-    rr3 = fmaf(h3, w.x, rr3); ri3 = fmaf(h3, w.y, ri3);
-    rr4 = fmaf(h4, w.x, rr4); ri4 = fmaf(h4, w.y, ri4);
-  }
-  for (int d = 0; d < 64; ++d) {
+    #pragma unroll
+    for (int k = 0; k < 5; ++k) {
+      float hv = hs[k][s];
+      rr[k] = fmaf(hv, w.x, rr[k]);
+      ri[k] = fmaf(hv, w.y, ri[k]);
+    }
+  }
+  #pragma unroll
+  for (int k = 0; k < 5; ++k) {
+    ps[sq][rl][k]     = rr[k];
+    ps[sq][rl][5 + k] = ri[k];
+  }
+  __syncthreads();
+
+  float Rr[5], Ri[5];
+  #pragma unroll
+  for (int k = 0; k < 5; ++k) {
+    Rr[k] = ps[0][rl][k] + ps[1][rl][k] + ps[2][rl][k] + ps[3][rl][k];
+    Ri[k] = ps[0][rl][5+k] + ps[1][rl][5+k] + ps[2][rl][5+k] + ps[3][rl][5+k];
+  }
+  const int d0 = sq * 16;
+  for (int dd = 0; dd < 16; ++dd) {
+    int d = d0 + dd;
     float w0r = wds[0][d][0], w0i = wds[0][d][1];
     float w1r = wds[1][d][0], w1i = wds[1][d][1];
     float w2r = wds[2][d][0], w2i = wds[2][d][1];
     float w3r = wds[3][d][0], w3i = wds[3][d][1];
     float s0v = S0[d], s1v = S1[d];
-    float rdr = rr0*w0r + rr1*w1r + rr2*s0v + rr3*w2r + rr4*w3r
-              - ri0*w0i - ri1*w1i - ri2*s1v - ri3*w2i - ri4*w3i;
-    float rdi = rr0*w0i + rr1*w1i + rr2*s1v + rr3*w2i + rr4*w3i
-              + ri0*w0r + ri1*w1r + ri2*s0v + ri3*w2r + ri4*w3r;
+    float rdr = Rr[0]*w0r + Rr[1]*w1r + Rr[2]*s0v + Rr[3]*w2r + Rr[4]*w3r
+              - Ri[0]*w0i - Ri[1]*w1i - Ri[2]*s1v - Ri[3]*w2i - Ri[4]*w3i;
+    float rdi = Rr[0]*w0i + Rr[1]*w1i + Rr[2]*s1v + Rr[3]*w2i + Rr[4]*w3i
+              + Ri[0]*w0r + Ri[1]*w1r + Ri[2]*s0v + Ri[3]*w2r + Ri[4]*w3r;
     float mag = sqrtf(rdr*rdr + rdi*rdi) * (1.0f / 16384.0f);
     int v = (d == 0) ? 0 : (d == 1) ? 1 : (d <= 61) ? 2 : ((d == 62) ? 3 : 4);
     float o = hs[v][r] + 0.1f * mag;
@@ -533,13 +565,13 @@
                                      rd2_w, rd2_b, rd2_s, rd2_t,
                                      up1_w, up1_b, up1_s, up1_t,
                                      up2_w, up2_b, up2_s, up2_t, ws);
-  k_front<<<1024, 256, 0, stream>>>(x, ws, ws + OFF_A);
-  k_cc1<<<1024, 256, 0, stream>>>(ws + OFF_A, ws + OFF_WCC1, ws + OFF_P);
+  k_front<<<2048, 128, 0, stream>>>(x, ws, ws + OFF_A);
+  k_cc1<<<1024, 128, 0, stream>>>(ws + OFF_A, ws + OFF_WCC1, ws + OFF_P);
   k_mid<<<512, 256, 0, stream>>>(ws + OFF_P, ws + OFF_BCC1,
                                  ws + OFF_WCC2, ws + OFF_BCC2,
                                  ws + OFF_WRD1, ws + OFF_BRD1,
                                  ws + OFF_WRD2, ws + OFF_BRD2, ws + OFF_R);
-  k_up1<<<512, 192, 0, stream>>>(ws + OFF_R, ws + OFF_WUP1, ws + OFF_BUP1, ws + OFF_U1);
-  k_up2<<<512, 192, 0, stream>>>(ws + OFF_U1, ws + OFF_WUP2, ws + OFF_BUP2, up3_w, up3_b, ws + OFF_H);
-  k_spec<<<64, 64, 0, stream>>>(ws + OFF_H, wr, wd, out);
-}
+  k_up<<<512, 192, 0, stream>>>(ws + OFF_R, ws + OFF_WUP1, ws + OFF_BUP1,
+                                ws + OFF_WUP2, ws + OFF_BUP2, up3_w, up3_b, ws + OFF_H);
+  k_spec<<<64, 256, 0, stream>>>(ws + OFF_H, wr, wd, out);
+}
```

New measurement: 412.1 us. 4.9% more time.
